# Optimization experiments

Measured on AMD Instinct MI355X. Metric: run time of the kernel, lower is better.

## Reference

```python
import jax, jax.numpy as jnp
import numpy as np

D_MODEL = 1024
N_HEADS = 16
D_K = D_MODEL // N_HEADS


def setup_inputs() -> dict:
    key = jax.random.key(0)
    ks = jax.random.split(key, 9)
    s = 1.0 / np.sqrt(D_MODEL)
    x = jax.random.normal(ks[0], (2, 2048, D_MODEL), dtype=jnp.float32)
    Wq = jax.random.uniform(ks[1], (D_MODEL, D_MODEL), jnp.float32, -s, s)
    bq = jax.random.uniform(ks[2], (D_MODEL,), jnp.float32, -s, s)
    Wk = jax.random.uniform(ks[3], (D_MODEL, D_MODEL), jnp.float32, -s, s)
    bk = jax.random.uniform(ks[4], (D_MODEL,), jnp.float32, -s, s)
    Wv = jax.random.uniform(ks[5], (D_MODEL, D_MODEL), jnp.float32, -s, s)
    bv = jax.random.uniform(ks[6], (D_MODEL,), jnp.float32, -s, s)
    Wo = jax.random.uniform(ks[7], (D_MODEL, D_MODEL), jnp.float32, -s, s)
    bo = jax.random.uniform(ks[8], (D_MODEL,), jnp.float32, -s, s)
    return {"x": x, "Wq": Wq, "bq": bq, "Wk": Wk, "bk": bk,
            "Wv": Wv, "bv": bv, "Wo": Wo, "bo": bo}


def reference(x, Wq, bq, Wk, bk, Wv, bv, Wo, bo):
    B, S, _ = x.shape
    # torch Linear: y = x @ W.T + b
    def proj(W, b):
        h = x @ W.T + b                       # [B,S,D]
        return h.reshape(B, S, N_HEADS, D_K).transpose(0, 2, 1, 3)  # [B,H,S,dk]
    Q, K, V = proj(Wq, bq), proj(Wk, bk), proj(Wv, bv)
    scale = 1.0 / np.sqrt(D_K).astype(np.float32)
    scores = jnp.einsum('bhqd,bhkd->bhqk', Q, K) * scale  # [B,H,S,S]
    causal = jnp.tril(jnp.ones((S, S), dtype=bool))
    scores = jnp.where(causal, scores, -jnp.inf)
    attn = jax.nn.softmax(scores, axis=-1)
    ctx = jnp.einsum('bhqk,bhkd->bhqd', attn, V)          # [B,H,S,dk]
    ctx = ctx.transpose(0, 2, 1, 3).reshape(B, S, D_MODEL)
    return ctx @ Wo.T + bo
```

## Files before the change

kernel.cpp:

```cpp
#include <hip/hip_runtime.h>
#include <stdint.h>

#define D_MODEL 1024
#define NHEADS  16
#define DKH     64
#define BATCH   2
#define SEQ     2048
#define NTOK    (BATCH*SEQ)

typedef unsigned short u16;
typedef __attribute__((ext_vector_type(8))) short short8;
typedef __attribute__((ext_vector_type(4))) float f32x4;
typedef __attribute__((ext_vector_type(16))) float f32x16;
typedef __attribute__((ext_vector_type(2))) unsigned int u32x2;
typedef __attribute__((address_space(1))) unsigned int as1_u32;
typedef __attribute__((address_space(3))) unsigned int as3_u32;

__device__ __forceinline__ u16 f2bf(float f) {
  unsigned int i = __float_as_uint(f);
  i += 0x7FFF + ((i >> 16) & 1);
  return (u16)(i >> 16);
}
__device__ __forceinline__ f32x4 mfma_bf16(short8 a, short8 b, f32x4 c) {
  return __builtin_amdgcn_mfma_f32_16x16x32_bf16(a, b, c, 0, 0, 0);
}
__device__ __forceinline__ f32x16 mfma32(short8 a, short8 b, f32x16 c) {
  return __builtin_amdgcn_mfma_f32_32x32x16_bf16(a, b, c, 0, 0, 0);
}
__device__ __forceinline__ void gload_lds16(const u16* g, u16* l) {
  __builtin_amdgcn_global_load_lds((as1_u32*)g, (as3_u32*)l, 16, 0, 0);
}
__device__ __forceinline__ short8 ld_frag(const u16* p) {
  short8 v; __builtin_memcpy(&v, __builtin_assume_aligned(p, 16), 16); return v;
}
__device__ __forceinline__ uint32_t pk_bf16_trunc(float hi, float lo) {
  return __builtin_amdgcn_perm(__float_as_uint(hi), __float_as_uint(lo), 0x07060302u);
}

#define QSCALE 0.18033688011112042f
#define M0LOG2 4.32808512266689f

__global__ __launch_bounds__(256)
void convert_kernel(const float* __restrict__ x,  const float* __restrict__ wq,
                    const float* __restrict__ wk, const float* __restrict__ wv,
                    const float* __restrict__ wo,
                    u16* __restrict__ xb,  u16* __restrict__ wqb,
                    u16* __restrict__ wkb, u16* __restrict__ wvb,
                    u16* __restrict__ wob)
{
  const int q = blockIdx.x * 256 + threadIdx.x;
  const float* src; u16* dst; int local;
  if (q < 1048576) { src = x; dst = xb; local = q; }
  else {
    const int t = q - 1048576, r = t >> 18;
    local = t & 262143;
    src = (r == 0) ? wq : (r == 1) ? wk : (r == 2) ? wv : wo;
    dst = (r == 0) ? wqb : (r == 1) ? wkb : (r == 2) ? wvb : wob;
  }
  float f[4];
  __builtin_memcpy(f, src + (size_t)local * 4, 16);
  uint32_t o[2];
  o[0] = ((uint32_t)f2bf(f[1]) << 16) | f2bf(f[0]);
  o[1] = ((uint32_t)f2bf(f[3]) << 16) | f2bf(f[2]);
  __builtin_memcpy(dst + (size_t)local * 4, o, 8);
}

__device__ __forceinline__ void gemm_core_bf16(
    const u16* __restrict__ A, const u16* __restrict__ Bt,
    int m0, int n0, u16* As, u16* Bs, f32x4 (&acc)[4][4])
{
  const int tid  = threadIdx.x;
  const int wave = tid >> 6, lane = tid & 63;
  const int quad = lane >> 4, l15 = lane & 15;
  const int wm = wave & 1, wn = wave >> 1;
  const int srow = lane >> 2;
  const int scol = (lane & 3) << 3;

#pragma unroll
  for (int i = 0; i < 4; i++)
#pragma unroll
    for (int j = 0; j < 4; j++) acc[i][j] = (f32x4){0.f, 0.f, 0.f, 0.f};

  for (int k0 = 0; k0 < D_MODEL; k0 += 32) {
    __syncthreads();
#pragma unroll
    for (int is = 0; is < 2; is++) {
      const int rbase = (is * 4 + wave) * 16;
      gload_lds16(A  + (size_t)(m0 + rbase + srow) * D_MODEL + k0 + scol, As + rbase * 32);
      gload_lds16(Bt + (size_t)(n0 + rbase + srow) * D_MODEL + k0 + scol, Bs + rbase * 32);
    }
    __syncthreads();

    short8 aF[4], bF[4];
#pragma unroll
    for (int i = 0; i < 4; i++)
      aF[i] = ld_frag(As + (wm * 64 + i * 16 + l15) * 32 + quad * 8);
#pragma unroll
    for (int j = 0; j < 4; j++)
      bF[j] = ld_frag(Bs + (wn * 64 + j * 16 + l15) * 32 + quad * 8);
#pragma unroll
    for (int i = 0; i < 4; i++)
#pragma unroll
      for (int j = 0; j < 4; j++)
        acc[i][j] = mfma_bf16(aF[i], bF[j], acc[i][j]);
  }
}

__global__ __launch_bounds__(512)
void qkv_fused_kernel(const u16* __restrict__ xb,
                      const u16* __restrict__ Wqb, const u16* __restrict__ Wkb,
                      const u16* __restrict__ Wvb,
                      const float* __restrict__ bq, const float* __restrict__ bk,
                      const float* __restrict__ bv,
                      u16* __restrict__ qplane, u16* __restrict__ kplane,
                      u16* __restrict__ vplane)
{
  __shared__ __align__(16) u16 SM[32768];
  u16* As = SM;
  u16* Bq = SM + 8192;
  u16* Bk = SM + 16384;
  u16* Bv = SM + 24576;

  const int m0 = blockIdx.x * 128;
  const int n0 = blockIdx.y * 128;

  const int tid  = threadIdx.x;
  const int wave = tid >> 6, lane = tid & 63;
  const int quad = lane >> 4, l15 = lane & 15;
  const int wm = wave & 1;
  const int wn = wave >> 1;
  const int srow = lane >> 2;
  const int scol = (lane & 3) << 3;
  const int wrow = wave * 16 + srow;
  const int ldso = wave * 512;

  const u16* srcA = xb  + (size_t)(m0 + wrow) * D_MODEL + scol;
  const u16* srcQ = Wqb + (size_t)(n0 + wrow) * D_MODEL + scol;
  const u16* srcK = Wkb + (size_t)(n0 + wrow) * D_MODEL + scol;
  const u16* srcV = Wvb + (size_t)(n0 + wrow) * D_MODEL + scol;

  f32x4 accQ[4][2], accK[4][2], accV[4][2];
#pragma unroll
  for (int i = 0; i < 4; i++)
#pragma unroll
    for (int j = 0; j < 2; j++) {
      accQ[i][j] = (f32x4){0.f, 0.f, 0.f, 0.f};
      accK[i][j] = (f32x4){0.f, 0.f, 0.f, 0.f};
      accV[i][j] = (f32x4){0.f, 0.f, 0.f, 0.f};
    }

  gload_lds16(srcA, As + ldso);
  gload_lds16(srcQ, Bq + ldso);
  gload_lds16(srcK, Bk + ldso);
  gload_lds16(srcV, Bv + ldso);
  __syncthreads();

  for (int k0 = 0; k0 < D_MODEL; k0 += 32) {
    const int buf = (k0 >> 5) & 1;
    if (k0 + 32 < D_MODEL) {
      const int nb = (buf ^ 1) * 4096 + ldso;
      gload_lds16(srcA + k0 + 32, As + nb);
      gload_lds16(srcQ + k0 + 32, Bq + nb);
      gload_lds16(srcK + k0 + 32, Bk + nb);
      gload_lds16(srcV + k0 + 32, Bv + nb);
    }
    const int bo = buf * 4096;
    short8 aF[4];
#pragma unroll
    for (int i = 0; i < 4; i++)
      aF[i] = ld_frag(As + bo + (wm * 64 + i * 16 + l15) * 32 + quad * 8);
    {
      const short8 b0 = ld_frag(Bq + bo + (wn * 32 + l15) * 32 + quad * 8);
      const short8 b1 = ld_frag(Bq + bo + (wn * 32 + 16 + l15) * 32 + quad * 8);
#pragma unroll
      for (int i = 0; i < 4; i++) {
        accQ[i][0] = mfma_bf16(aF[i], b0, accQ[i][0]);
        accQ[i][1] = mfma_bf16(aF[i], b1, accQ[i][1]);
      }
    }
    {
      const short8 b0 = ld_frag(Bk + bo + (wn * 32 + l15) * 32 + quad * 8);
      const short8 b1 = ld_frag(Bk + bo + (wn * 32 + 16 + l15) * 32 + quad * 8);
#pragma unroll
      for (int i = 0; i < 4; i++) {
        accK[i][0] = mfma_bf16(aF[i], b0, accK[i][0]);
        accK[i][1] = mfma_bf16(aF[i], b1, accK[i][1]);
      }
    }
    {
      const short8 b0 = ld_frag(Bv + bo + (wn * 32 + l15) * 32 + quad * 8);
      const short8 b1 = ld_frag(Bv + bo + (wn * 32 + 16 + l15) * 32 + quad * 8);
#pragma unroll
      for (int i = 0; i < 4; i++) {
        accV[i][0] = mfma_bf16(aF[i], b0, accV[i][0]);
        accV[i][1] = mfma_bf16(aF[i], b1, accV[i][1]);
      }
    }
    __syncthreads();
  }

  u16* KStg = SM;
  u16* VStg = SM + 16384;
  const int t4 = ((wn >> 1) * 2 + wm) * 4096;

#pragma unroll
  for (int j = 0; j < 2; j++) {
    const int gcol = n0 + wn * 32 + j * 16 + l15;
    const int dj = gcol & 63;
    const float bkv = bk[gcol];
    const float bvv = bv[gcol];
    const int vswz = (dj & 7) << 3;
#pragma unroll
    for (int i = 0; i < 4; i++) {
#pragma unroll
      for (int r = 0; r < 4; r++) {
        const int rr = i * 16 + quad * 4 + r;
        KStg[t4 + rr * 64 + (dj ^ ((rr & 7) << 3))] = f2bf(accK[i][j][r] + bkv);
      }
      const int kkb = i * 16 + quad * 4;
      uint32_t w2[2];
      w2[0] = ((uint32_t)f2bf(accV[i][j][1] + bvv) << 16) | f2bf(accV[i][j][0] + bvv);
      w2[1] = ((uint32_t)f2bf(accV[i][j][3] + bvv) << 16) | f2bf(accV[i][j][2] + bvv);
      __builtin_memcpy(__builtin_assume_aligned(
          VStg + t4 + dj * 64 + (kkb ^ vswz), 8), w2, 8);
    }
  }
  __syncthreads();

#pragma unroll
  for (int j = 0; j < 2; j++) {
    const int gcol = n0 + wn * 32 + j * 16 + l15;
    const float bqv = bq[gcol];
    const int h = gcol >> 6, dj = gcol & 63;
#pragma unroll
    for (int i = 0; i < 4; i++) {
#pragma unroll
      for (int r = 0; r < 4; r++) {
        const int grow = m0 + wm * 64 + i * 16 + quad * 4 + r;
        const int b = grow >> 11, s = grow & (SEQ - 1);
        qplane[(((size_t)(b * NHEADS + h)) * SEQ + s) * DKH + dj] =
            f2bf((accQ[i][j][r] + bqv) * QSCALE);
      }
    }
  }

  const int hh = (wave & 3) >> 1, tt = wave & 1;
  const int b  = m0 >> 11;
  const int h  = (n0 >> 6) + hh;
  const int kt = ((m0 & (SEQ - 1)) >> 6) + tt;
  u16* gdst = ((wave < 4) ? kplane : vplane)
              + (((size_t)(b * NHEADS + h)) * 32 + kt) * 4096;
  const u16* lsrc = SM + wave * 4096;
#pragma unroll
  for (int ps = 0; ps < 8; ps++) {
    uint32_t tmp[4];
    __builtin_memcpy(tmp, __builtin_assume_aligned(lsrc + ps * 512 + lane * 8, 16), 16);
    __builtin_memcpy(__builtin_assume_aligned(gdst + ps * 512 + lane * 8, 16), tmp, 16);
  }
}


__device__ __forceinline__ void soft_pack(const f32x16& s, const int khBase,
                                          const bool diag, const int qloc,
                                          const int h4, float& l_acc,
                                          short8& fA, short8& fB) {
  float pv[16];
#pragma unroll
  for (int rr = 0; rr < 16; rr++) {
    float v = exp2f(s[rr]);
    if (diag) {
      const int kloc = khBase + (rr & 3) + 8 * (rr >> 2) + h4;
      if (kloc > qloc) v = 0.f;
    }
    pv[rr] = v;
  }
  const float t0 = (pv[0] + pv[1]) + (pv[2] + pv[3]);
  const float t1 = (pv[4] + pv[5]) + (pv[6] + pv[7]);
  const float t2 = (pv[8] + pv[9]) + (pv[10] + pv[11]);
  const float t3 = (pv[12] + pv[13]) + (pv[14] + pv[15]);
  l_acc += (t0 + t1) + (t2 + t3);
  uint32_t w[2][4];
#pragma unroll
  for (int ks = 0; ks < 2; ks++) {
    const uint32_t x0 = pk_bf16_trunc(pv[8 * ks + 1], pv[8 * ks + 0]);
    const uint32_t x1 = pk_bf16_trunc(pv[8 * ks + 3], pv[8 * ks + 2]);
    const uint32_t y0 = pk_bf16_trunc(pv[8 * ks + 5], pv[8 * ks + 4]);
    const uint32_t y1 = pk_bf16_trunc(pv[8 * ks + 7], pv[8 * ks + 6]);
    const u32x2 r0 = __builtin_amdgcn_permlane32_swap(x0, y0, false, false);
    const u32x2 r1 = __builtin_amdgcn_permlane32_swap(x1, y1, false, false);
    w[ks][0] = r0[0]; w[ks][1] = r1[0]; w[ks][2] = r0[1]; w[ks][3] = r1[1];
  }
  __builtin_memcpy(&fA, &w[0][0], 16);
  __builtin_memcpy(&fB, &w[1][0], 16);
}

__device__ __forceinline__ void osum_write(float* OS, const f32x16& o0,
                                           const f32x16& o1, int qb, int l31) {
#pragma unroll
  for (int rr = 0; rr < 16; rr++) {
    const int q = qb + (rr & 3) + 8 * (rr >> 2);
    OS[q * 64 + l31]      = o0[rr];
    OS[q * 64 + 32 + l31] = o1[rr];
  }
}
__device__ __forceinline__ void osum_add(const float* OS, f32x16& o0,
                                         f32x16& o1, int qb, int l31) {
#pragma unroll
  for (int rr = 0; rr < 16; rr++) {
    const int q = qb + (rr & 3) + 8 * (rr >> 2);
    o0[rr] += OS[q * 64 + l31];
    o1[rr] += OS[q * 64 + 32 + l31];
  }
}

__device__ __forceinline__ void stage_tile(const u16* gsrc, u16* ldst,
                                           int w4, int lane8) {
#pragma unroll
  for (int i = 0; i < 2; i++) {
    const int chunk = (w4 * 2 + i) * 512;
    gload_lds16(gsrc + chunk + lane8, ldst + chunk);
  }
}

__global__ __launch_bounds__(512, 4)
void attn_kernel(const u16* __restrict__ Qp, const u16* __restrict__ Kp,
                 const u16* __restrict__ Vp, u16* __restrict__ ctx)
{
  __shared__ __align__(16) u16 Ks[2][2][4096];
  __shared__ __align__(16) u16 Vts[2][2][4096];

  const int xp = blockIdx.x;
  const int bh = blockIdx.y;
  const u16* Q  = Qp + (size_t)bh * SEQ * DKH;
  const u16* Kt = Kp + (size_t)bh * SEQ * DKH;
  const u16* Vt = Vp + (size_t)bh * SEQ * DKH;

  const int tid  = threadIdx.x;
  const int w    = tid >> 6;
  const int lane = tid & 63;
  const int lane8 = lane * 8;
  const int l31  = lane & 31, h = lane >> 5, h8 = h * 8;
  const int g    = w >> 2;
  const int w4   = w & 3;
  const int wq   = (w >> 1) & 1;
  const int kh   = w & 1;
  const int pg   = g * 2 + kh;
  const int b = bh >> 4, hd = bh & 15;
  const int qloc = wq * 32 + l31;
  const int qb   = wq * 32 + h * 4;
  const int xr   = (l31 & 7) << 3;
  const int khB  = kh * 32;

  float* Osum0 = (float*)&Ks[0][0][0];
  float* Osum1 = (float*)&Ks[1][0][0];
  float* Ls    = (float*)&Vts[0][0][0];

#pragma unroll
  for (int p = 0; p < 2; p++) {
    const int qt = p ? xp : 31 - xp;
    const int q0 = qt * 64;
    const int maxR = (qt >> 1) + 1;

    const u16* qrow = Q + (size_t)(q0 + qloc) * DKH + h8;
    const short8 qf0 = ld_frag(qrow + 0);
    const short8 qf1 = ld_frag(qrow + 16);
    const short8 qf2 = ld_frag(qrow + 32);
    const short8 qf3 = ld_frag(qrow + 48);

    __syncthreads();
    const bool act0 = (g <= qt);
    if (act0) {
      stage_tile(Kt + (size_t)g * 4096, &Ks[g][0][0],  w4, lane8);
      stage_tile(Vt + (size_t)g * 4096, &Vts[g][0][0], w4, lane8);
    }
    float l_acc = 0.f;
    f32x16 oacc0, oacc1;
#pragma unroll
    for (int rr = 0; rr < 16; rr++) { oacc0[rr] = 0.f; oacc1[rr] = 0.f; }
    __syncthreads();

    for (int r = 0; r < maxR; r++) {
      const int kt = 2 * r + g;
      const int buf = r & 1;
      const bool act = (kt <= qt);
      if (kt + 2 <= qt) {
        stage_tile(Kt + (size_t)(kt + 2) * 4096, &Ks[g][buf ^ 1][0],  w4, lane8);
        stage_tile(Vt + (size_t)(kt + 2) * 4096, &Vts[g][buf ^ 1][0], w4, lane8);
      }
      if (act) {
        f32x16 s;
#pragma unroll
        for (int rr = 0; rr < 16; rr++) s[rr] = -M0LOG2;
        const u16* kbase = &Ks[g][buf][0] + (size_t)(khB + l31) * 64;
        s = mfma32(ld_frag(kbase + ((0  + h8) ^ xr)), qf0, s);
        s = mfma32(ld_frag(kbase + ((16 + h8) ^ xr)), qf1, s);
        s = mfma32(ld_frag(kbase + ((32 + h8) ^ xr)), qf2, s);
        s = mfma32(ld_frag(kbase + ((48 + h8) ^ xr)), qf3, s);
        short8 pa0, pa1;
        soft_pack(s, khB, kt == qt, qloc, h * 4, l_acc, pa0, pa1);
        const u16* v0 = &Vts[g][buf][0] + (size_t)l31 * 64;
        const u16* v1 = &Vts[g][buf][0] + (size_t)(32 + l31) * 64;
        oacc0 = mfma32(pa0, ld_frag(v0 + ((khB + 0  + h8) ^ xr)), oacc0);
        oacc1 = mfma32(pa0, ld_frag(v1 + ((khB + 0  + h8) ^ xr)), oacc1);
        oacc0 = mfma32(pa1, ld_frag(v0 + ((khB + 16 + h8) ^ xr)), oacc0);
        oacc1 = mfma32(pa1, ld_frag(v1 + ((khB + 16 + h8) ^ xr)), oacc1);
      }
      __syncthreads();
    }

    l_acc += __shfl_xor(l_acc, 32);
    if (lane < 32) Ls[pg * 64 + wq * 32 + l31] = l_acc;
    if (pg == 1) osum_write(Osum0, oacc0, oacc1, qb, l31);
    if (pg == 3) osum_write(Osum1, oacc0, oacc1, qb, l31);
    __syncthreads();
    if (pg == 0) osum_add(Osum0, oacc0, oacc1, qb, l31);
    if (pg == 2) osum_add(Osum1, oacc0, oacc1, qb, l31);
    if (w == 1) {
      const float sum = Ls[lane] + Ls[64 + lane] + Ls[128 + lane] + Ls[192 + lane];
      Ls[lane] = 1.f / sum;
    }
    __syncthreads();
    if (pg == 2) osum_write(Osum0, oacc0, oacc1, qb, l31);
    __syncthreads();
    if (pg == 0) {
#pragma unroll
      for (int rr = 0; rr < 16; rr++) {
        const int q = qb + (rr & 3) + 8 * (rr >> 2);
        const float linv = Ls[q];
        u16* dst = ctx + ((size_t)(b * SEQ + q0 + q)) * D_MODEL + hd * DKH;
        dst[l31]      = f2bf((oacc0[rr] + Osum0[q * 64 + l31]) * linv);
        dst[32 + l31] = f2bf((oacc1[rr] + Osum0[q * 64 + 32 + l31]) * linv);
      }
    }
  }
}

__global__ __launch_bounds__(256)
void oproj_kernel(const u16* __restrict__ ctx, const u16* __restrict__ Wob,
                  const float* __restrict__ bo, float* __restrict__ out)
{
  __shared__ __align__(16) u16 As[128 * 32];
  __shared__ __align__(16) u16 Bs[128 * 32];
  const int m0 = blockIdx.x * 128, n0 = blockIdx.y * 128;

  f32x4 acc[4][4];
  gemm_core_bf16(ctx, Wob, m0, n0, As, Bs, acc);

  const int tid = threadIdx.x, wave = tid >> 6, lane = tid & 63;
  const int quad = lane >> 4, l15 = lane & 15;
  const int wm = wave & 1, wn = wave >> 1;
#pragma unroll
  for (int j = 0; j < 4; j++) {
    const int gcol = n0 + wn * 64 + j * 16 + l15;
    const float bias_v = bo[gcol];
#pragma unroll
    for (int i = 0; i < 4; i++) {
#pragma unroll
      for (int r = 0; r < 4; r++) {
        const int grow = m0 + wm * 64 + i * 16 + quad * 4 + r;
        out[(size_t)grow * D_MODEL + gcol] = acc[i][j][r] + bias_v;
      }
    }
  }
}

extern "C" void kernel_launch(void* const* d_in, const int* in_sizes, int n_in,
                              void* d_out, int out_size, void* d_ws, size_t ws_size,
                              hipStream_t stream) {
  const float* x  = (const float*)d_in[0];
  const float* Wq = (const float*)d_in[1];
  const float* bq = (const float*)d_in[2];
  const float* Wk = (const float*)d_in[3];
  const float* bk = (const float*)d_in[4];
  const float* Wv = (const float*)d_in[5];
  const float* bv = (const float*)d_in[6];
  const float* Wo = (const float*)d_in[7];
  const float* bo = (const float*)d_in[8];
  u16*   ws   = (u16*)d_ws;
  u16*   o16  = (u16*)d_out;
  float* out  = (float*)d_out;

  const size_t plane = (size_t)NTOK * D_MODEL;
  u16* Kp  = ws;
  u16* Vp  = ws + plane;
  u16* xb  = ws + 2 * plane;
  u16* ctx = ws + 2 * plane;
  u16* Wob = ws + 3 * plane;
  u16* Qp  = o16;
  u16* Wqb = o16 + 4 * 1048576;
  u16* Wkb = o16 + 5 * 1048576;
  u16* Wvb = o16 + 6 * 1048576;

  convert_kernel<<<dim3(8192), dim3(256), 0, stream>>>(x, Wq, Wk, Wv, Wo,
                                                       xb, Wqb, Wkb, Wvb, Wob);
  qkv_fused_kernel<<<dim3(32, 8), dim3(512), 0, stream>>>(xb, Wqb, Wkb, Wvb,
                                                          bq, bk, bv, Qp, Kp, Vp);
  attn_kernel<<<dim3(16, 32), dim3(512), 0, stream>>>(Qp, Kp, Vp, ctx);
  oproj_kernel<<<dim3(32, 8), dim3(256), 0, stream>>>(ctx, Wob, bo, out);
}
```

Before: 196.4 us.

## Enlarge attention query tile to 128 rows with 16-wave blocks

The attention kernel now processes 128-query tiles per pass using 1024-thread blocks (16 waves), with each wave covering a full 64-key tile instead of half. Each staged K/V tile is therefore reused by twice as many queries, which cuts LDS staging traffic and the number of barrier rounds per query. Causal masking is generalized with per-wave activity and mask checks, and s_setprio is placed around the MFMA groups to favor matrix issue. The grid halves to 256 blocks, which may leave compute units underutilized, and the larger blocks raise per-block register and occupancy pressure.

```diff
diff --git a/kernel.cpp b/kernel.cpp
--- a/kernel.cpp
+++ b/kernel.cpp
@@ -261,16 +261,16 @@
 
 
 __device__ __forceinline__ void soft_pack(const f32x16& s, const int khBase,
-                                          const bool diag, const int qloc,
+                                          const bool needMask, const int qrel,
                                           const int h4, float& l_acc,
                                           short8& fA, short8& fB) {
   float pv[16];
 #pragma unroll
   for (int rr = 0; rr < 16; rr++) {
     float v = exp2f(s[rr]);
-    if (diag) {
+    if (needMask) {
       const int kloc = khBase + (rr & 3) + 8 * (rr >> 2) + h4;
-      if (kloc > qloc) v = 0.f;
+      if (kloc > qrel) v = 0.f;
     }
     pv[rr] = v;
   }
@@ -313,21 +313,13 @@
   }
 }
 
-__device__ __forceinline__ void stage_tile(const u16* gsrc, u16* ldst,
-                                           int w4, int lane8) {
-#pragma unroll
-  for (int i = 0; i < 2; i++) {
-    const int chunk = (w4 * 2 + i) * 512;
-    gload_lds16(gsrc + chunk + lane8, ldst + chunk);
-  }
-}
-
-__global__ __launch_bounds__(512, 4)
+__global__ __launch_bounds__(1024, 4)
 void attn_kernel(const u16* __restrict__ Qp, const u16* __restrict__ Kp,
                  const u16* __restrict__ Vp, u16* __restrict__ ctx)
 {
   __shared__ __align__(16) u16 Ks[2][2][4096];
   __shared__ __align__(16) u16 Vts[2][2][4096];
+  __shared__ float Ls[512];
 
   const int xp = blockIdx.x;
   const int bh = blockIdx.y;
@@ -338,41 +330,37 @@
   const int tid  = threadIdx.x;
   const int w    = tid >> 6;
   const int lane = tid & 63;
-  const int lane8 = lane * 8;
   const int l31  = lane & 31, h = lane >> 5, h8 = h * 8;
-  const int g    = w >> 2;
-  const int w4   = w & 3;
-  const int wq   = (w >> 1) & 1;
-  const int kh   = w & 1;
-  const int pg   = g * 2 + kh;
+  const int wq   = w >> 2;
+  const int g    = (w >> 1) & 1;
+  const int pg   = w & 3;
+  const int w8   = ((w >> 2) << 1) | (w & 1);
+  const int sbase = w8 * 512 + lane * 8;
   const int b = bh >> 4, hd = bh & 15;
-  const int qloc = wq * 32 + l31;
-  const int qb   = wq * 32 + h * 4;
-  const int xr   = (l31 & 7) << 3;
-  const int khB  = kh * 32;
+  const int qq = wq * 32 + l31;
+  const int qb = wq * 32 + h * 4;
+  const int xr = (l31 & 7) << 3;
+  const int h4 = h * 4;
 
   float* Osum0 = (float*)&Ks[0][0][0];
-  float* Osum1 = (float*)&Ks[1][0][0];
-  float* Ls    = (float*)&Vts[0][0][0];
+  float* Osum1 = (float*)&Vts[0][0][0];
 
 #pragma unroll
   for (int p = 0; p < 2; p++) {
-    const int qt = p ? xp : 31 - xp;
-    const int q0 = qt * 64;
-    const int maxR = (qt >> 1) + 1;
-
-    const u16* qrow = Q + (size_t)(q0 + qloc) * DKH + h8;
+    const int qt = p ? xp : 15 - xp;
+    const int q0 = qt * 128;
+    const int maxR = qt + 1;
+    const int ktmax = 2 * qt + 1;
+
+    const u16* qrow = Q + (size_t)(q0 + qq) * DKH + h8;
     const short8 qf0 = ld_frag(qrow + 0);
     const short8 qf1 = ld_frag(qrow + 16);
     const short8 qf2 = ld_frag(qrow + 32);
     const short8 qf3 = ld_frag(qrow + 48);
 
     __syncthreads();
-    const bool act0 = (g <= qt);
-    if (act0) {
-      stage_tile(Kt + (size_t)g * 4096, &Ks[g][0][0],  w4, lane8);
-      stage_tile(Vt + (size_t)g * 4096, &Vts[g][0][0], w4, lane8);
-    }
+    gload_lds16(Kt + (size_t)g * 4096 + sbase, &Ks[g][0][0] + sbase);
+    gload_lds16(Vt + (size_t)g * 4096 + sbase, &Vts[g][0][0] + sbase);
     float l_acc = 0.f;
     f32x16 oacc0, oacc1;
 #pragma unroll
@@ -382,42 +370,73 @@
     for (int r = 0; r < maxR; r++) {
       const int kt = 2 * r + g;
       const int buf = r & 1;
-      const bool act = (kt <= qt);
-      if (kt + 2 <= qt) {
-        stage_tile(Kt + (size_t)(kt + 2) * 4096, &Ks[g][buf ^ 1][0],  w4, lane8);
-        stage_tile(Vt + (size_t)(kt + 2) * 4096, &Vts[g][buf ^ 1][0], w4, lane8);
-      }
+      if (kt + 2 <= ktmax) {
+        gload_lds16(Kt + (size_t)(kt + 2) * 4096 + sbase, &Ks[g][buf ^ 1][0] + sbase);
+        gload_lds16(Vt + (size_t)(kt + 2) * 4096 + sbase, &Vts[g][buf ^ 1][0] + sbase);
+      }
+      const int dd = kt * 64 - q0 + qt * 0;
+      const int ddr = kt * 64 - 128 * qt;
+      const bool act = (ddr <= wq * 32 + 31);
       if (act) {
-        f32x16 s;
-#pragma unroll
-        for (int rr = 0; rr < 16; rr++) s[rr] = -M0LOG2;
-        const u16* kbase = &Ks[g][buf][0] + (size_t)(khB + l31) * 64;
-        s = mfma32(ld_frag(kbase + ((0  + h8) ^ xr)), qf0, s);
-        s = mfma32(ld_frag(kbase + ((16 + h8) ^ xr)), qf1, s);
-        s = mfma32(ld_frag(kbase + ((32 + h8) ^ xr)), qf2, s);
-        s = mfma32(ld_frag(kbase + ((48 + h8) ^ xr)), qf3, s);
-        short8 pa0, pa1;
-        soft_pack(s, khB, kt == qt, qloc, h * 4, l_acc, pa0, pa1);
-        const u16* v0 = &Vts[g][buf][0] + (size_t)l31 * 64;
-        const u16* v1 = &Vts[g][buf][0] + (size_t)(32 + l31) * 64;
-        oacc0 = mfma32(pa0, ld_frag(v0 + ((khB + 0  + h8) ^ xr)), oacc0);
-        oacc1 = mfma32(pa0, ld_frag(v1 + ((khB + 0  + h8) ^ xr)), oacc1);
-        oacc0 = mfma32(pa1, ld_frag(v0 + ((khB + 16 + h8) ^ xr)), oacc0);
-        oacc1 = mfma32(pa1, ld_frag(v1 + ((khB + 16 + h8) ^ xr)), oacc1);
-      }
+        const bool needMask = (ddr + 63 > wq * 32);
+        const int qrel = qq - ddr;
+        const u16* ksb = &Ks[g][buf][0];
+        const u16* vtb = &Vts[g][buf][0];
+        short8 pa0, pa1, pa2, pa3;
+        {
+          f32x16 s;
+#pragma unroll
+          for (int rr = 0; rr < 16; rr++) s[rr] = -M0LOG2;
+          const u16* kb0 = ksb + (size_t)l31 * 64;
+          __builtin_amdgcn_s_setprio(1);
+          s = mfma32(ld_frag(kb0 + ((0  + h8) ^ xr)), qf0, s);
+          s = mfma32(ld_frag(kb0 + ((16 + h8) ^ xr)), qf1, s);
+          s = mfma32(ld_frag(kb0 + ((32 + h8) ^ xr)), qf2, s);
+          s = mfma32(ld_frag(kb0 + ((48 + h8) ^ xr)), qf3, s);
+          __builtin_amdgcn_s_setprio(0);
+          soft_pack(s, 0, needMask, qrel, h4, l_acc, pa0, pa1);
+        }
+        {
+          f32x16 s;
+#pragma unroll
+          for (int rr = 0; rr < 16; rr++) s[rr] = -M0LOG2;
+          const u16* kb1 = ksb + (size_t)(32 + l31) * 64;
+          __builtin_amdgcn_s_setprio(1);
+          s = mfma32(ld_frag(kb1 + ((0  + h8) ^ xr)), qf0, s);
+          s = mfma32(ld_frag(kb1 + ((16 + h8) ^ xr)), qf1, s);
+          s = mfma32(ld_frag(kb1 + ((32 + h8) ^ xr)), qf2, s);
+          s = mfma32(ld_frag(kb1 + ((48 + h8) ^ xr)), qf3, s);
+          __builtin_amdgcn_s_setprio(0);
+          soft_pack(s, 32, needMask, qrel, h4, l_acc, pa2, pa3);
+        }
+        const u16* v0 = vtb + (size_t)l31 * 64;
+        const u16* v1 = vtb + (size_t)(32 + l31) * 64;
+        __builtin_amdgcn_s_setprio(1);
+        oacc0 = mfma32(pa0, ld_frag(v0 + ((0  + h8) ^ xr)), oacc0);
+        oacc1 = mfma32(pa0, ld_frag(v1 + ((0  + h8) ^ xr)), oacc1);
+        oacc0 = mfma32(pa1, ld_frag(v0 + ((16 + h8) ^ xr)), oacc0);
+        oacc1 = mfma32(pa1, ld_frag(v1 + ((16 + h8) ^ xr)), oacc1);
+        oacc0 = mfma32(pa2, ld_frag(v0 + ((32 + h8) ^ xr)), oacc0);
+        oacc1 = mfma32(pa2, ld_frag(v1 + ((32 + h8) ^ xr)), oacc1);
+        oacc0 = mfma32(pa3, ld_frag(v0 + ((48 + h8) ^ xr)), oacc0);
+        oacc1 = mfma32(pa3, ld_frag(v1 + ((48 + h8) ^ xr)), oacc1);
+        __builtin_amdgcn_s_setprio(0);
+      }
+      (void)dd;
       __syncthreads();
     }
 
     l_acc += __shfl_xor(l_acc, 32);
-    if (lane < 32) Ls[pg * 64 + wq * 32 + l31] = l_acc;
+    if (lane < 32) Ls[pg * 128 + wq * 32 + l31] = l_acc;
     if (pg == 1) osum_write(Osum0, oacc0, oacc1, qb, l31);
     if (pg == 3) osum_write(Osum1, oacc0, oacc1, qb, l31);
     __syncthreads();
     if (pg == 0) osum_add(Osum0, oacc0, oacc1, qb, l31);
     if (pg == 2) osum_add(Osum1, oacc0, oacc1, qb, l31);
-    if (w == 1) {
-      const float sum = Ls[lane] + Ls[64 + lane] + Ls[128 + lane] + Ls[192 + lane];
-      Ls[lane] = 1.f / sum;
+    if (pg == 1 && wq < 2) {
+      const int q = wq * 64 + lane;
+      const float s4 = Ls[q] + Ls[128 + q] + Ls[256 + q] + Ls[384 + q];
+      Ls[q] = 1.f / s4;
     }
     __syncthreads();
     if (pg == 2) osum_write(Osum0, oacc0, oacc1, qb, l31);
@@ -495,6 +514,6 @@
                                                        xb, Wqb, Wkb, Wvb, Wob);
   qkv_fused_kernel<<<dim3(32, 8), dim3(512), 0, stream>>>(xb, Wqb, Wkb, Wvb,
                                                           bq, bk, bv, Qp, Kp, Vp);
-  attn_kernel<<<dim3(16, 32), dim3(512), 0, stream>>>(Qp, Kp, Vp, ctx);
+  attn_kernel<<<dim3(8, 32), dim3(1024), 0, stream>>>(Qp, Kp, Vp, ctx);
   oproj_kernel<<<dim3(32, 8), dim3(256), 0, stream>>>(ctx, Wob, bo, out);
 }
```

After: 232.9 us. 1.19x slower.

## Double-buffer LDS and use 8 waves in output projection GEMM

Applied to the files above, without the earlier changes.

Rewrites the output projection kernel to use 512 threads (8 waves, each computing a 64x32 sub-tile) and double-buffered LDS staging. The next k-slice's global-to-LDS loads are issued before the current slice's MFMAs, and only one barrier is kept per iteration. This aims to hide global load latency and raise wave occupancy, at the cost of twice the LDS per block and fewer MFMAs per wave per loaded fragment.

```diff
diff --git a/kernel.cpp b/kernel.cpp
--- a/kernel.cpp
+++ b/kernel.cpp
@@ -65,47 +65,6 @@
   __builtin_memcpy(dst + (size_t)local * 4, o, 8);
 }
 
-__device__ __forceinline__ void gemm_core_bf16(
-    const u16* __restrict__ A, const u16* __restrict__ Bt,
-    int m0, int n0, u16* As, u16* Bs, f32x4 (&acc)[4][4])
-{
-  const int tid  = threadIdx.x;
-  const int wave = tid >> 6, lane = tid & 63;
-  const int quad = lane >> 4, l15 = lane & 15;
-  const int wm = wave & 1, wn = wave >> 1;
-  const int srow = lane >> 2;
-  const int scol = (lane & 3) << 3;
-
-#pragma unroll
-  for (int i = 0; i < 4; i++)
-#pragma unroll
-    for (int j = 0; j < 4; j++) acc[i][j] = (f32x4){0.f, 0.f, 0.f, 0.f};
-
-  for (int k0 = 0; k0 < D_MODEL; k0 += 32) {
-    __syncthreads();
-#pragma unroll
-    for (int is = 0; is < 2; is++) {
-      const int rbase = (is * 4 + wave) * 16;
-      gload_lds16(A  + (size_t)(m0 + rbase + srow) * D_MODEL + k0 + scol, As + rbase * 32);
-      gload_lds16(Bt + (size_t)(n0 + rbase + srow) * D_MODEL + k0 + scol, Bs + rbase * 32);
-    }
-    __syncthreads();
-
-    short8 aF[4], bF[4];
-#pragma unroll
-    for (int i = 0; i < 4; i++)
-      aF[i] = ld_frag(As + (wm * 64 + i * 16 + l15) * 32 + quad * 8);
-#pragma unroll
-    for (int j = 0; j < 4; j++)
-      bF[j] = ld_frag(Bs + (wn * 64 + j * 16 + l15) * 32 + quad * 8);
-#pragma unroll
-    for (int i = 0; i < 4; i++)
-#pragma unroll
-      for (int j = 0; j < 4; j++)
-        acc[i][j] = mfma_bf16(aF[i], bF[j], acc[i][j]);
-  }
-}
-
 __global__ __launch_bounds__(512)
 void qkv_fused_kernel(const u16* __restrict__ xb,
                       const u16* __restrict__ Wqb, const u16* __restrict__ Wkb,
@@ -435,23 +394,65 @@
   }
 }
 
-__global__ __launch_bounds__(256)
+__global__ __launch_bounds__(512)
 void oproj_kernel(const u16* __restrict__ ctx, const u16* __restrict__ Wob,
                   const float* __restrict__ bo, float* __restrict__ out)
 {
-  __shared__ __align__(16) u16 As[128 * 32];
-  __shared__ __align__(16) u16 Bs[128 * 32];
-  const int m0 = blockIdx.x * 128, n0 = blockIdx.y * 128;
-
-  f32x4 acc[4][4];
-  gemm_core_bf16(ctx, Wob, m0, n0, As, Bs, acc);
-
-  const int tid = threadIdx.x, wave = tid >> 6, lane = tid & 63;
+  __shared__ __align__(16) u16 SM[16384];
+  u16* As = SM;
+  u16* Bs = SM + 8192;
+
+  const int m0 = blockIdx.x * 128;
+  const int n0 = blockIdx.y * 128;
+
+  const int tid  = threadIdx.x;
+  const int wave = tid >> 6, lane = tid & 63;
   const int quad = lane >> 4, l15 = lane & 15;
-  const int wm = wave & 1, wn = wave >> 1;
-#pragma unroll
-  for (int j = 0; j < 4; j++) {
-    const int gcol = n0 + wn * 64 + j * 16 + l15;
+  const int wm = wave & 1;
+  const int wn = wave >> 1;
+  const int srow = lane >> 2;
+  const int scol = (lane & 3) << 3;
+  const int wrow = wave * 16 + srow;
+  const int ldso = wave * 512;
+
+  const u16* srcA = ctx + (size_t)(m0 + wrow) * D_MODEL + scol;
+  const u16* srcB = Wob + (size_t)(n0 + wrow) * D_MODEL + scol;
+
+  f32x4 acc[4][2];
+#pragma unroll
+  for (int i = 0; i < 4; i++)
+#pragma unroll
+    for (int j = 0; j < 2; j++) acc[i][j] = (f32x4){0.f, 0.f, 0.f, 0.f};
+
+  gload_lds16(srcA, As + ldso);
+  gload_lds16(srcB, Bs + ldso);
+  __syncthreads();
+
+  for (int k0 = 0; k0 < D_MODEL; k0 += 32) {
+    const int buf = (k0 >> 5) & 1;
+    if (k0 + 32 < D_MODEL) {
+      const int nb = (buf ^ 1) * 4096 + ldso;
+      gload_lds16(srcA + k0 + 32, As + nb);
+      gload_lds16(srcB + k0 + 32, Bs + nb);
+    }
+    const int bo2 = buf * 4096;
+    short8 aF[4];
+#pragma unroll
+    for (int i = 0; i < 4; i++)
+      aF[i] = ld_frag(As + bo2 + (wm * 64 + i * 16 + l15) * 32 + quad * 8);
+    const short8 b0 = ld_frag(Bs + bo2 + (wn * 32 + l15) * 32 + quad * 8);
+    const short8 b1 = ld_frag(Bs + bo2 + (wn * 32 + 16 + l15) * 32 + quad * 8);
+#pragma unroll
+    for (int i = 0; i < 4; i++) {
+      acc[i][0] = mfma_bf16(aF[i], b0, acc[i][0]);
+      acc[i][1] = mfma_bf16(aF[i], b1, acc[i][1]);
+    }
+    __syncthreads();
+  }
+
+#pragma unroll
+  for (int j = 0; j < 2; j++) {
+    const int gcol = n0 + wn * 32 + j * 16 + l15;
     const float bias_v = bo[gcol];
 #pragma unroll
     for (int i = 0; i < 4; i++) {
@@ -496,5 +497,5 @@
   qkv_fused_kernel<<<dim3(32, 8), dim3(512), 0, stream>>>(xb, Wqb, Wkb, Wvb,
                                                           bq, bk, bv, Qp, Kp, Vp);
   attn_kernel<<<dim3(16, 32), dim3(512), 0, stream>>>(Qp, Kp, Vp, ctx);
-  oproj_kernel<<<dim3(32, 8), dim3(256), 0, stream>>>(ctx, Wob, bo, out);
-}
+  oproj_kernel<<<dim3(32, 8), dim3(512), 0, stream>>>(ctx, Wob, bo, out);
+}
```

After: 192.9 us. Within noise of the previous version (-1.8%).
